# Kernel optimization log

Hardware: AMD Instinct MI355X
Metric: run time of the kernel (lower is better)

The kernel has to match this reference:

```python
import jax, jax.numpy as jnp
import numpy as np

B, T, N, HOR = 64, 12, 1024, 12
D_IN, D_OUT, RNN, E, K = 1, 1, 64, 8, 3
MEM_N, MEM_D = 10, 32
DEC = RNN + MEM_D  # 96 (memory_type='local')
YCOV = 1


def setup_inputs() -> dict:
    key = jax.random.key(0)
    ks = jax.random.split(key, 12)
    s = 0.1  # xavier-ish scale for weights
    return {
        "x": jax.random.normal(ks[0], (B, T, N, D_IN), jnp.float32),
        "y_cov": jax.random.normal(ks[1], (B, HOR, N, YCOV), jnp.float32),
        "node_embeddings": jax.random.normal(ks[2], (N, E), jnp.float32),
        "enc_gate_W": jax.random.normal(ks[3], (K * (D_IN + RNN), 2 * RNN), jnp.float32) * s,
        "enc_gate_b": jnp.zeros((2 * RNN,), jnp.float32),
        "enc_up_W": jax.random.normal(ks[4], (K * (D_IN + RNN), RNN), jnp.float32) * s,
        "enc_up_b": jnp.zeros((RNN,), jnp.float32),
        "Memory": jax.random.normal(ks[5], (MEM_N, MEM_D), jnp.float32) * s,
        "Wq": jax.random.normal(ks[6], (RNN, MEM_D), jnp.float32) * s,
        "FC_E": jax.random.normal(ks[7], (MEM_D, E), jnp.float32) * s,
        "dec_gate_W": jax.random.normal(ks[8], (K * (D_OUT + YCOV + DEC), 2 * DEC), jnp.float32) * s,
        "dec_gate_b": jnp.zeros((2 * DEC,), jnp.float32),
        "dec_up_W": jax.random.normal(ks[9], (K * (D_OUT + YCOV + DEC), DEC), jnp.float32) * s,
        "dec_up_b": jnp.zeros((DEC,), jnp.float32),
        "proj_W": jax.random.normal(ks[10], (DEC, D_OUT), jnp.float32) * s,
        "proj_b": jnp.zeros((D_OUT,), jnp.float32),
    }


def _cheb_supports(S):
    # S: (N,N) soft adjacency -> stacked Chebyshev set [I, S, 2S@S_{k-1}-S_{k-2}, ...], (K,N,N)
    n = S.shape[0]
    sup = [jnp.eye(n, dtype=S.dtype), S]
    for _ in range(2, K):
        sup.append(2.0 * S @ sup[-1] - sup[-2])
    return jnp.stack(sup)


def _agcn(xin, supports, W, b):
    # xin: (B,N,C); supports: (K,N,N); W: (K*C, O)
    xg = jnp.einsum('knm,bmc->bnkc', supports, xin)  # k-major matches torch cat order
    bsz, n = xin.shape[0], xin.shape[1]
    xg = xg.reshape(bsz, n, -1)
    return xg @ W + b


def _cell(xt, state, supports, gW, gb, uW, ub, hdim):
    inp = jnp.concatenate([xt, state], axis=-1)
    z_r = jax.nn.sigmoid(_agcn(inp, supports, gW, gb))
    z, r = z_r[..., :hdim], z_r[..., hdim:]
    cand = jnp.concatenate([xt, z * state], axis=-1)
    hc = jnp.tanh(_agcn(cand, supports, uW, ub))
    return r * state + (1.0 - r) * hc


def reference(x, y_cov, node_embeddings, enc_gate_W, enc_gate_b, enc_up_W, enc_up_b,
              Memory, Wq, FC_E, dec_gate_W, dec_gate_b, dec_up_W, dec_up_b, proj_W, proj_b):
    # ---- encoder supports from static node embeddings (2D path in AGCN) ----
    S_enc = jax.nn.softmax(jax.nn.relu(node_embeddings @ node_embeddings.T), axis=1)
    sup_enc = _cheb_supports(S_enc)

    # ---- encoder: GRU-style recurrence over T timesteps (lax.scan) ----
    def enc_step(state, xt):
        h = _cell(xt, state, sup_enc, enc_gate_W, enc_gate_b, enc_up_W, enc_up_b, RNN)
        return h, None
    h0 = jnp.zeros((x.shape[0], N, RNN), x.dtype)
    h_t, _ = jax.lax.scan(enc_step, h0, jnp.swapaxes(x, 0, 1))  # final hidden (B,N,RNN)

    # ---- memory query (memory_type='local') ----
    query = h_t @ Wq                                  # (B,N,MEM_D)
    att = jax.nn.softmax(query @ Memory.T, axis=-1)   # (B,N,MEM_N)
    proto_t = att @ Memory                            # (B,N,MEM_D)
    W_E = proto_t @ FC_E                              # (B,N,E) meta node embeddings

    # ---- decoder supports from meta embeddings (3D path: einsum sums over batch) ----
    S_dec = jax.nn.softmax(jax.nn.relu(jnp.einsum('bnc,bmc->nm', W_E, W_E)), axis=1)
    sup_dec = _cheb_supports(S_dec)

    # ---- stepwise decoder with go symbol ----
    dec_h0 = jnp.concatenate([h_t, proto_t], axis=-1)  # (B,N,DEC)
    go0 = jnp.zeros((x.shape[0], N, D_OUT), x.dtype)

    def dec_step(carry, yc_t):
        go, state = carry
        xt = jnp.concatenate([go, yc_t], axis=-1)
        h = _cell(xt, state, sup_dec, dec_gate_W, dec_gate_b, dec_up_W, dec_up_b, DEC)
        go_new = h @ proj_W + proj_b
        return (go_new, h), go_new

    _, outs = jax.lax.scan(dec_step, (go0, dec_h0), jnp.swapaxes(y_cov, 0, 1))
    return jnp.swapaxes(outs, 0, 1)  # (B, horizon, N, D_OUT)
```

## Files before the change

kernel.cpp:

```cpp
#include <hip/hip_runtime.h>
#include <hip/hip_bf16.h>

constexpr int B_ = 64, T_ = 12, NN = 1024, HOR_ = 12;

typedef __attribute__((ext_vector_type(8))) short short8;
typedef __attribute__((ext_vector_type(4))) float f32x4;
typedef unsigned short ushort_t;

static __device__ inline ushort_t f2bh(float v) {
  __hip_bfloat16 h = __float2bfloat16(v);
  return *reinterpret_cast<ushort_t*>(&h);
}
static __device__ inline float bh2f(ushort_t u) {
  __hip_bfloat16 h = *reinterpret_cast<__hip_bfloat16*>(&u);
  return __bfloat162float(h);
}
static __device__ inline void split_bf16(float v, ushort_t& hi, ushort_t& lo) {
  hi = f2bh(v);
  lo = f2bh(v - bh2f(hi));
}

static __device__ inline void gload_lds16(const ushort_t* g, ushort_t* l) {
  __builtin_amdgcn_global_load_lds(
      (const __attribute__((address_space(1))) unsigned int*)g,
      (__attribute__((address_space(3))) unsigned int*)l, 16, 0, 0);
}

__global__ void gemm_nt_kernel(const float* __restrict__ A, const float* __restrict__ Bm,
                               float* __restrict__ C, int Ncol, int Kd) {
  __shared__ float As[16][68];
  __shared__ float Bs[16][68];
  const int bm = blockIdx.y * 64, bn = blockIdx.x * 64;
  const int tid = threadIdx.x;
  const int tx = tid & 15, ty = tid >> 4;
  float acc[4][4] = {};
  for (int k0 = 0; k0 < Kd; k0 += 16) {
#pragma unroll
    for (int r = 0; r < 4; ++r) {
      const int m = (tid >> 4) + r * 16;
      const int kk = tid & 15;
      const int k = k0 + kk;
      As[kk][m] = (k < Kd) ? A[(size_t)(bm + m) * Kd + k] : 0.f;
      Bs[kk][m] = (k < Kd) ? Bm[(size_t)(bn + m) * Kd + k] : 0.f;
    }
    __syncthreads();
#pragma unroll
    for (int kk = 0; kk < 16; ++kk) {
      float a[4], b[4];
#pragma unroll
      for (int i = 0; i < 4; ++i) a[i] = As[kk][ty * 4 + i];
#pragma unroll
      for (int j = 0; j < 4; ++j) b[j] = Bs[kk][tx * 4 + j];
#pragma unroll
      for (int i = 0; i < 4; ++i)
#pragma unroll
        for (int j = 0; j < 4; ++j) acc[i][j] += a[i] * b[j];
    }
    __syncthreads();
  }
#pragma unroll
  for (int i = 0; i < 4; ++i)
#pragma unroll
    for (int j = 0; j < 4; ++j)
      C[(size_t)(bm + ty * 4 + i) * Ncol + bn + tx * 4 + j] = acc[i][j];
}

__global__ void relu_softmax_kernel(float* __restrict__ S, ushort_t* __restrict__ Sh,
                                    ushort_t* __restrict__ Sl) {
  const int row = blockIdx.x;
  float* r = S + (size_t)row * NN;
  const int tid = threadIdx.x;
  float v[4];
  float mx = 0.f;
#pragma unroll
  for (int j = 0; j < 4; ++j) {
    float xv = fmaxf(r[tid + j * 256], 0.f);
    v[j] = xv;
    mx = fmaxf(mx, xv);
  }
#pragma unroll
  for (int off = 1; off < 64; off <<= 1) mx = fmaxf(mx, __shfl_xor(mx, off));
  __shared__ float sred[4];
  const int wv = tid >> 6;
  if ((tid & 63) == 0) sred[wv] = mx;
  __syncthreads();
  mx = fmaxf(fmaxf(sred[0], sred[1]), fmaxf(sred[2], sred[3]));
  __syncthreads();
  float s = 0.f;
#pragma unroll
  for (int j = 0; j < 4; ++j) { v[j] = expf(v[j] - mx); s += v[j]; }
#pragma unroll
  for (int off = 1; off < 64; off <<= 1) s += __shfl_xor(s, off);
  if ((tid & 63) == 0) sred[wv] = s;
  __syncthreads();
  s = sred[0] + sred[1] + sred[2] + sred[3];
  const float inv = 1.f / s;
#pragma unroll
  for (int j = 0; j < 4; ++j) {
    const float sv = v[j] * inv;
    const size_t e = (size_t)row * NN + tid + j * 256;
    r[tid + j * 256] = sv;
    ushort_t hi, lo;
    split_bf16(sv, hi, lo);
    Sh[e] = hi;
    Sl[e] = lo;
  }
}

__global__ void st_kernel(const float* __restrict__ S, ushort_t* __restrict__ STh,
                          ushort_t* __restrict__ STl) {
  __shared__ float tile[64][65];
  const int bx = blockIdx.x * 64, by = blockIdx.y * 64;
  const int tid = threadIdx.x;
  const int cl = tid & 63, rq = tid >> 6;
#pragma unroll
  for (int r = 0; r < 16; ++r) {
    const int rr = rq + r * 4;
    tile[rr][cl] = S[(size_t)(by + rr) * NN + bx + cl];
  }
  __syncthreads();
#pragma unroll
  for (int r = 0; r < 16; ++r) {
    const int rr = rq + r * 4;
    const float v = tile[cl][rr];
    ushort_t hi, lo;
    split_bf16(v, hi, lo);
    STh[(size_t)(bx + rr) * NN + by + cl] = hi;
    STl[(size_t)(bx + rr) * NN + by + cl] = lo;
  }
}

__global__ void cheb_mfma_kernel(const ushort_t* __restrict__ S1h,
                                 const ushort_t* __restrict__ S1l,
                                 const ushort_t* __restrict__ STh,
                                 const ushort_t* __restrict__ STl,
                                 ushort_t* __restrict__ Mh) {
  __shared__ __align__(16) ushort_t sA[2 * 32 * 64];
  __shared__ __align__(16) ushort_t sB[2 * 64 * 64];
  const int bj = blockIdx.x * 64, bn = blockIdx.y * 32;
  const int tid = threadIdx.x;
  const int w = tid >> 6, lane = tid & 63;
  const int row = lane & 15, kq = lane >> 4;
  const int srow8 = lane >> 3, sslot = lane & 7;
  f32x4 acc[2] = {};
  for (int k0 = 0; k0 < NN; k0 += 64) {
#pragma unroll
    for (int t2 = 0; t2 < 2; ++t2) {
      const int c = w + t2 * 4, p = c >> 2, i = c & 3;
      const int grow = i * 8 + srow8;
      const int gch = sslot ^ (grow & 7);
      const ushort_t* src = (p ? S1l : S1h) + (size_t)(bn + grow) * NN + k0 + gch * 8;
      gload_lds16(src, sA + p * 2048 + i * 512);
    }
#pragma unroll
    for (int t2 = 0; t2 < 4; ++t2) {
      const int c2 = w + t2 * 4, p = c2 >> 3, rb = c2 & 7;
      const int grow = rb * 8 + srow8;
      const int gch = sslot ^ (grow & 7);
      const ushort_t* src = (p ? STl : STh) + (size_t)(bj + grow) * NN + k0 + gch * 8;
      gload_lds16(src, sB + p * 4096 + rb * 512);
    }
    __syncthreads();
#pragma unroll
    for (int kk = 0; kk < 2; ++kk) {
      const int rB = w * 16 + row;
      const int chB = ((kk * 4 + kq) ^ (rB & 7)) * 8;
      const short8 bh = *(const short8*)(sB + rB * 64 + chB);
      const short8 bl = *(const short8*)(sB + 4096 + rB * 64 + chB);
#pragma unroll
      for (int mt = 0; mt < 2; ++mt) {
        const int rA = mt * 16 + row;
        const int chA = ((kk * 4 + kq) ^ (rA & 7)) * 8;
        const short8 ah = *(const short8*)(sA + rA * 64 + chA);
        const short8 al = *(const short8*)(sA + 2048 + rA * 64 + chA);
        acc[mt] = __builtin_amdgcn_mfma_f32_16x16x32_bf16(ah, bh, acc[mt], 0, 0, 0);
        acc[mt] = __builtin_amdgcn_mfma_f32_16x16x32_bf16(ah, bl, acc[mt], 0, 0, 0);
        acc[mt] = __builtin_amdgcn_mfma_f32_16x16x32_bf16(al, bh, acc[mt], 0, 0, 0);
      }
    }
    __syncthreads();
  }
  const int j = bj + w * 16 + row;
#pragma unroll
  for (int mt = 0; mt < 2; ++mt) {
    const int node0 = bn + mt * 16 + kq * 4;
#pragma unroll
    for (int r = 0; r < 4; ++r)
      Mh[(size_t)(node0 + r) * NN + j] = f2bh(2.f * acc[mt][r]);
  }
}

__global__ void wt_kernel(const float* __restrict__ W, ushort_t* __restrict__ Wth,
                          int KK, int NO, int KP, int NOP) {
  const int e = blockIdx.x * 256 + threadIdx.x;
  if (e >= NOP * KP) return;
  const int no = e / KP, k = e - no * KP;
  const float v = (no < NO && k < KK) ? W[(size_t)k * NO + no] : 0.f;
  Wth[e] = f2bh(v);
}

template <int C, int KP, int MODE>
__global__ void prep_kernel(const float* __restrict__ src0, const float* __restrict__ src1,
                            const float* __restrict__ hst,
                            ushort_t* __restrict__ Agh, ushort_t* __restrict__ XTh) {
  __shared__ float tile[64][65];
  const int bj = blockIdx.x * 64, bn = blockIdx.y * 64;
  const int tid = threadIdx.x;
  const int jl = tid & 63, nq = tid >> 6;
  const int j = bj + jl;
  const int b = j / C, c = j - b * C;
#pragma unroll
  for (int r = 0; r < 16; ++r) {
    const int node = bn + nq + r * 4;
    const int idx = node * 64 + b;
    float v;
    if (MODE == 0) {
      v = (c == 0) ? src0[((size_t)b * T_) * NN + node]
                   : hst[(size_t)idx * 64 + (c - 1)];
    } else {
      v = (c == 0) ? src0[idx]
        : (c == 1) ? src1[((size_t)b * HOR_) * NN + node]
                   : hst[(size_t)idx * 96 + (c - 2)];
    }
    tile[nq + r * 4][jl] = v;
    Agh[(size_t)idx * KP + c] = f2bh(v);
  }
  __syncthreads();
  const int nl = tid & 63, jq = tid >> 6;
#pragma unroll
  for (int r = 0; r < 16; ++r) {
    const int jj = bj + jq + r * 4;
    XTh[(size_t)jj * NN + bn + nl] = f2bh(tile[nl][jq + r * 4]);
  }
}

template <int C, int KP>
__global__ void xt_kernel(const ushort_t* __restrict__ Agh, ushort_t* __restrict__ XTh) {
  __shared__ ushort_t tile[64][70];
  const int bj = blockIdx.x * 64, bn = blockIdx.y * 64;
  const int tid = threadIdx.x;
  const int jl = tid & 63, nq = tid >> 6;
  const int j = bj + jl;
  const int b = j / C, c = j - b * C;
#pragma unroll
  for (int r = 0; r < 16; ++r) {
    const int node = bn + nq + r * 4;
    tile[nq + r * 4][jl] = Agh[(size_t)(node * 64 + b) * KP + c];
  }
  __syncthreads();
  const int nl = tid & 63, jq = tid >> 6;
#pragma unroll
  for (int r = 0; r < 16; ++r) {
    const int jj = bj + jq + r * 4;
    XTh[(size_t)jj * NN + bn + nl] = tile[nl][jq + r * 4];
  }
}

__global__ void set_x_kernel(const float* __restrict__ x, ushort_t* __restrict__ Agh, int t) {
  const int idx = blockIdx.x * 256 + threadIdx.x;
  const int n = idx >> 6, b = idx & 63;
  Agh[(size_t)idx * 224] = f2bh(x[((size_t)b * T_ + t) * NN + n]);
}

template <int C, int KP>
__global__ void graph_mfma_kernel(const ushort_t* __restrict__ S1h,
                                  const ushort_t* __restrict__ Mh,
                                  const ushort_t* __restrict__ XTh,
                                  ushort_t* __restrict__ Agh) {
  constexpr int W = B_ * C;
  const int bj = blockIdx.x * 128;
  if (bj >= W) return;
  __shared__ __align__(16) ushort_t sA[2 * 32 * 64];
  __shared__ __align__(16) ushort_t sB[128 * 64];
  const int bn = blockIdx.y * 32;
  const int tid = threadIdx.x;
  const int w = tid >> 6, lane = tid & 63;
  const int row = lane & 15, kq = lane >> 4;
  const int srow8 = lane >> 3;
  const int sslot = lane & 7;

  const int s = w >> 1;
  const int jhalf = (w & 1) * 64;
  const ushort_t* A_lds = sA + s * (32 * 64);

  f32x4 acc[2][4] = {};
  for (int k0 = 0; k0 < NN; k0 += 64) {
#pragma unroll
    for (int t2 = 0; t2 < 6; ++t2) {
      const int cid = w + t2 * 4;
      if (cid < 8) {
        const int p = cid >> 2, i = cid & 3;
        const int grow = i * 8 + srow8;
        const int gch = sslot ^ (grow & 7);
        const ushort_t* g = (p ? Mh : S1h) + (size_t)(bn + grow) * NN + k0 + gch * 8;
        gload_lds16(g, sA + p * (32 * 64) + i * 512);
      } else {
        const int rb = cid - 8;
        const int brow = rb * 8 + srow8;
        const int gch = sslot ^ (brow & 7);
        const ushort_t* g = XTh + (size_t)(bj + brow) * NN + k0 + gch * 8;
        gload_lds16(g, sB + rb * 512);
      }
    }
    __syncthreads();
    short8 a[2][2];
#pragma unroll
    for (int kk = 0; kk < 2; ++kk)
#pragma unroll
      for (int mt = 0; mt < 2; ++mt) {
        const int r = mt * 16 + row;
        const int chunk = (kk * 4 + kq) ^ (r & 7);
        a[kk][mt] = *(const short8*)(A_lds + r * 64 + chunk * 8);
      }
#pragma unroll
    for (int nt = 0; nt < 4; ++nt) {
#pragma unroll
      for (int kk = 0; kk < 2; ++kk) {
        const int r = jhalf + nt * 16 + row;
        const int chunk = (kk * 4 + kq) ^ (r & 7);
        const short8 bh = *(const short8*)(sB + r * 64 + chunk * 8);
#pragma unroll
        for (int mt = 0; mt < 2; ++mt)
          acc[mt][nt] = __builtin_amdgcn_mfma_f32_16x16x32_bf16(a[kk][mt], bh, acc[mt][nt], 0, 0, 0);
      }
    }
    __syncthreads();
  }
  const int slice_off = (s + 1) * C;
#pragma unroll
  for (int nt = 0; nt < 4; ++nt) {
    const int j = bj + jhalf + nt * 16 + row;
    if (j < W) {
      const int b = j / C, c = j - b * C;
      const size_t coloff = (size_t)(slice_off + c);
#pragma unroll
      for (int mt = 0; mt < 2; ++mt) {
        const int node0 = bn + mt * 16 + kq * 4;
        float sub[4] = {0.f, 0.f, 0.f, 0.f};
        if (s == 1) {
          const ushort_t* xp = XTh + (size_t)j * NN + node0;
#pragma unroll
          for (int r = 0; r < 4; ++r) sub[r] = bh2f(xp[r]);
        }
#pragma unroll
        for (int r = 0; r < 4; ++r) {
          const size_t a = (size_t)((node0 + r) * 64 + b) * KP + coloff;
          Agh[a] = f2bh(acc[mt][nt][r] - sub[r]);
        }
      }
    }
  }
}

template <int KP, int NO, int NOP, int MODE, int H, int CO>
__global__ void dense_mfma_kernel(ushort_t* __restrict__ Agh,
                                  const ushort_t* __restrict__ Wth,
                                  const float* __restrict__ bias,
                                  float* __restrict__ hstate,
                                  float* __restrict__ rbuf) {
  constexpr int NFR = NO / 16;
  __shared__ __align__(16) ushort_t sAh[128 * 32];
  __shared__ __align__(16) ushort_t sBh[NOP * 32];
  const int row0 = blockIdx.x * 128;
  const int tid = threadIdx.x;
  const int w = tid >> 6, lane = tid & 63;
  const int col16 = lane & 15, four = lane >> 4;
  const int srow = lane >> 2;
  const int scol = ((lane & 3) ^ ((srow >> 1) & 3)) * 8;
  const int kqs = (four ^ ((col16 >> 1) & 3)) * 8;
  f32x4 acc[2][NFR] = {};
  for (int k0 = 0; k0 < KP; k0 += 32) {
    for (int c = w; c < 8; c += 4) {
      const size_t g = (size_t)(row0 + c * 16 + srow) * KP + k0 + scol;
      gload_lds16(Agh + g, sAh + c * 512);
    }
    for (int c = w; c < NOP / 16; c += 4) {
      const size_t g = (size_t)(c * 16 + srow) * KP + k0 + scol;
      gload_lds16(Wth + g, sBh + c * 512);
    }
    __syncthreads();
    short8 ah[2];
#pragma unroll
    for (int mt = 0; mt < 2; ++mt) {
      const int r = (w * 32 + mt * 16 + col16) * 32 + kqs;
      ah[mt] = *(const short8*)(sAh + r);
    }
#pragma unroll
    for (int nt = 0; nt < NFR; ++nt) {
      const int r = (nt * 16 + col16) * 32 + kqs;
      const short8 bh = *(const short8*)(sBh + r);
#pragma unroll
      for (int mt = 0; mt < 2; ++mt)
        acc[mt][nt] = __builtin_amdgcn_mfma_f32_16x16x32_bf16(ah[mt], bh, acc[mt][nt], 0, 0, 0);
    }
    __syncthreads();
  }
#pragma unroll
  for (int nt = 0; nt < NFR; ++nt) {
    const int col = nt * 16 + col16;
    const float bv = bias[col];
#pragma unroll
    for (int mt = 0; mt < 2; ++mt) {
      const int rbase = row0 + w * 32 + mt * 16 + four * 4;
#pragma unroll
      for (int r = 0; r < 4; ++r) {
        const int row = rbase + r;
        const float v = acc[mt][nt][r] + bv;
        if (MODE == 2) {
          const float sg = 1.f / (1.f + expf(-v));
          if (col < H) {
            const float hv = hstate[(size_t)row * H + col];
            Agh[(size_t)row * KP + CO + col] = f2bh(sg * hv);
          } else {
            rbuf[(size_t)row * H + (col - H)] = sg;
          }
        } else {
          const float rg = rbuf[(size_t)row * H + col];
          const float hv = hstate[(size_t)row * H + col];
          const float hnew = rg * hv + (1.f - rg) * tanhf(v);
          hstate[(size_t)row * H + col] = hnew;
          Agh[(size_t)row * KP + CO + col] = f2bh(hnew);
        }
      }
    }
  }
}

__global__ void attn_kernel(const float* __restrict__ h, const float* __restrict__ Wq,
                            const float* __restrict__ Mem, const float* __restrict__ FCE,
                            float* __restrict__ hB, float* __restrict__ WE) {
  __shared__ float sWq[64 * 32];
  __shared__ float sM[10 * 32];
  __shared__ float sF[32 * 8];
  const int tid = threadIdx.x;
  for (int i = tid; i < 64 * 32; i += 256) sWq[i] = Wq[i];
  for (int i = tid; i < 10 * 32; i += 256) sM[i] = Mem[i];
  for (int i = tid; i < 32 * 8; i += 256) sF[i] = FCE[i];
  __syncthreads();
  const int idx = blockIdx.x * 256 + tid;
  const float* hp = h + (size_t)idx * 64;
  float* hd = hB + (size_t)idx * 96;
  float q[32] = {};
  for (int i0 = 0; i0 < 16; ++i0) {
    const float4 h4 = *(const float4*)(hp + i0 * 4);
#pragma unroll
    for (int jj = 0; jj < 4; ++jj) {
      const float hv = ((const float*)&h4)[jj];
      hd[i0 * 4 + jj] = hv;
      const int i = i0 * 4 + jj;
#pragma unroll
      for (int c = 0; c < 32; ++c) q[c] += hv * sWq[i * 32 + c];
    }
  }
  float lg[10];
  float mx = -1e30f;
#pragma unroll
  for (int m = 0; m < 10; ++m) {
    float s = 0.f;
#pragma unroll
    for (int c = 0; c < 32; ++c) s += q[c] * sM[m * 32 + c];
    lg[m] = s;
    mx = fmaxf(mx, s);
  }
  float den = 0.f;
#pragma unroll
  for (int m = 0; m < 10; ++m) { lg[m] = expf(lg[m] - mx); den += lg[m]; }
  const float inv = 1.f / den;
  float p[32] = {};
#pragma unroll
  for (int m = 0; m < 10; ++m) {
    const float a = lg[m] * inv;
#pragma unroll
    for (int c = 0; c < 32; ++c) p[c] += a * sM[m * 32 + c];
  }
#pragma unroll
  for (int c = 0; c < 32; ++c) hd[64 + c] = p[c];
  float* wd = WE + (size_t)idx * 8;
#pragma unroll
  for (int e = 0; e < 8; ++e) {
    float s = 0.f;
#pragma unroll
    for (int c = 0; c < 32; ++c) s += p[c] * sF[c * 8 + e];
    wd[e] = s;
  }
}

__global__ void proj_kernel(const float* __restrict__ h, const float* __restrict__ pW,
                            const float* __restrict__ pb, float* __restrict__ go,
                            const float* __restrict__ ycov, ushort_t* __restrict__ Agh,
                            float* __restrict__ out, int t) {
  __shared__ float sW[96];
  if (threadIdx.x < 96) sW[threadIdx.x] = pW[threadIdx.x];
  __syncthreads();
  const int idx = blockIdx.x * 256 + threadIdx.x;
  const float* hp = h + (size_t)idx * 96;
  float acc = pb[0];
  for (int j0 = 0; j0 < 24; ++j0) {
    const float4 h4 = *(const float4*)(hp + j0 * 4);
    acc += h4.x * sW[j0 * 4] + h4.y * sW[j0 * 4 + 1] + h4.z * sW[j0 * 4 + 2] + h4.w * sW[j0 * 4 + 3];
  }
  go[idx] = acc;
  const int n = idx >> 6, b = idx & 63;
  out[((size_t)b * HOR_ + t) * NN + n] = acc;
  if (t + 1 < HOR_) {
    Agh[(size_t)idx * 320 + 0] = f2bh(acc);
    Agh[(size_t)idx * 320 + 1] = f2bh(ycov[((size_t)b * HOR_ + t + 1) * NN + n]);
  }
}

extern "C" void kernel_launch(void* const* d_in, const int* in_sizes, int n_in,
                              void* d_out, int out_size, void* d_ws, size_t ws_size,
                              hipStream_t stream) {
  const float* x    = (const float*)d_in[0];
  const float* ycov = (const float*)d_in[1];
  const float* emb  = (const float*)d_in[2];
  const float* egW  = (const float*)d_in[3];
  const float* egb  = (const float*)d_in[4];
  const float* euW  = (const float*)d_in[5];
  const float* eub  = (const float*)d_in[6];
  const float* Mem  = (const float*)d_in[7];
  const float* Wq   = (const float*)d_in[8];
  const float* FCE  = (const float*)d_in[9];
  const float* dgW  = (const float*)d_in[10];
  const float* dgb  = (const float*)d_in[11];
  const float* duW  = (const float*)d_in[12];
  const float* dub  = (const float*)d_in[13];
  const float* pW   = (const float*)d_in[14];
  const float* pb   = (const float*)d_in[15];
  float* out = (float*)d_out;

  char* w = (char*)d_ws;
  auto alloc = [&](size_t bytes) {
    void* p = (void*)w;
    w += (bytes + 255) & ~(size_t)255;
    return p;
  };
  float* S1   = (float*)alloc((size_t)NN * NN * 4);
  float* rbuf = (float*)alloc((size_t)NN * B_ * 96 * 4);
  float* hA   = (float*)alloc((size_t)NN * B_ * 64 * 4);
  float* hB   = (float*)alloc((size_t)NN * B_ * 96 * 4);
  float* go   = (float*)alloc((size_t)NN * B_ * 4);
  float* WE   = (float*)alloc((size_t)NN * B_ * 8 * 4);
  ushort_t* S1h = (ushort_t*)alloc((size_t)NN * NN * 2);
  ushort_t* S1l = (ushort_t*)alloc((size_t)NN * NN * 2);
  ushort_t* Mh  = (ushort_t*)alloc((size_t)NN * NN * 2);
  ushort_t* STh = (ushort_t*)alloc((size_t)NN * NN * 2);
  ushort_t* STl = (ushort_t*)alloc((size_t)NN * NN * 2);
  ushort_t* XTh = (ushort_t*)alloc((size_t)B_ * 98 * NN * 2);
  ushort_t* Agh = (ushort_t*)alloc((size_t)NN * B_ * 320 * 2);
  ushort_t* WtegH = (ushort_t*)alloc(128 * 224 * 2);
  ushort_t* WteuH = (ushort_t*)alloc(64 * 224 * 2);
  ushort_t* WtdgH = (ushort_t*)alloc(192 * 320 * 2);
  ushort_t* WtduH = (ushort_t*)alloc(128 * 320 * 2);
  (void)ws_size; (void)in_sizes; (void)n_in; (void)out_size;

  const dim3 blk(256);

  wt_kernel<<<(128 * 224 + 255) / 256, blk, 0, stream>>>(egW, WtegH, 195, 128, 224, 128);
  wt_kernel<<<(64 * 224 + 255) / 256, blk, 0, stream>>>(euW, WteuH, 195, 64, 224, 64);
  wt_kernel<<<(192 * 320 + 255) / 256, blk, 0, stream>>>(dgW, WtdgH, 294, 192, 320, 192);
  wt_kernel<<<(128 * 320 + 255) / 256, blk, 0, stream>>>(duW, WtduH, 294, 96, 320, 128);
  hipMemsetAsync(Agh, 0, (size_t)NN * B_ * 320 * 2, stream);
  hipMemsetAsync(hA, 0, (size_t)NN * B_ * 64 * 4, stream);
  hipMemsetAsync(go, 0, (size_t)NN * B_ * 4, stream);

  gemm_nt_kernel<<<dim3(16, 16), blk, 0, stream>>>(emb, emb, S1, NN, 8);
  relu_softmax_kernel<<<NN, blk, 0, stream>>>(S1, S1h, S1l);
  st_kernel<<<dim3(16, 16), blk, 0, stream>>>(S1, STh, STl);
  cheb_mfma_kernel<<<dim3(16, 32), blk, 0, stream>>>(S1h, S1l, STh, STl, Mh);

  for (int t = 0; t < T_; ++t) {
    if (t == 0) {
      prep_kernel<65, 224, 0><<<dim3(65, 16), blk, 0, stream>>>(x, nullptr, hA, Agh, XTh);
    } else {
      set_x_kernel<<<256, blk, 0, stream>>>(x, Agh, t);
      xt_kernel<65, 224><<<dim3(65, 16), blk, 0, stream>>>(Agh, XTh);
    }
    graph_mfma_kernel<65, 224><<<dim3(40, 32), blk, 0, stream>>>(S1h, Mh, XTh, Agh);
    dense_mfma_kernel<224, 128, 128, 2, 64, 1><<<512, blk, 0, stream>>>(Agh, WtegH, egb, hA, rbuf);
    xt_kernel<65, 224><<<dim3(65, 16), blk, 0, stream>>>(Agh, XTh);
    graph_mfma_kernel<65, 224><<<dim3(40, 32), blk, 0, stream>>>(S1h, Mh, XTh, Agh);
    dense_mfma_kernel<224, 64, 64, 1, 64, 1><<<512, blk, 0, stream>>>(Agh, WteuH, eub, hA, rbuf);
  }

  attn_kernel<<<256, blk, 0, stream>>>(hA, Wq, Mem, FCE, hB, WE);
  gemm_nt_kernel<<<dim3(16, 16), blk, 0, stream>>>(WE, WE, S1, NN, 512);
  relu_softmax_kernel<<<NN, blk, 0, stream>>>(S1, S1h, S1l);
  st_kernel<<<dim3(16, 16), blk, 0, stream>>>(S1, STh, STl);
  cheb_mfma_kernel<<<dim3(16, 32), blk, 0, stream>>>(S1h, S1l, STh, STl, Mh);

  for (int t = 0; t < HOR_; ++t) {
    if (t == 0) {
      prep_kernel<98, 320, 2><<<dim3(98, 16), blk, 0, stream>>>(go, ycov, hB, Agh, XTh);
    } else {
      xt_kernel<98, 320><<<dim3(98, 16), blk, 0, stream>>>(Agh, XTh);
    }
    graph_mfma_kernel<98, 320><<<dim3(56, 32), blk, 0, stream>>>(S1h, Mh, XTh, Agh);
    dense_mfma_kernel<320, 192, 192, 2, 96, 2><<<512, blk, 0, stream>>>(Agh, WtdgH, dgb, hB, rbuf);
    xt_kernel<98, 320><<<dim3(98, 16), blk, 0, stream>>>(Agh, XTh);
    graph_mfma_kernel<98, 320><<<dim3(56, 32), blk, 0, stream>>>(S1h, Mh, XTh, Agh);
    dense_mfma_kernel<320, 96, 128, 1, 96, 2><<<512, blk, 0, stream>>>(Agh, WtduH, dub, hB, rbuf);
    proj_kernel<<<256, blk, 0, stream>>>(hB, pW, pb, go, ycov, Agh, out, t);
  }
}
```

Measured before the change: 3.893 ms.

## Fuse x-load into transpose, projection into update GEMM, and use MFMA SYRK

Folds set_x into the transpose kernel and the output projection into the decoder update GEMM epilogue via a lane shuffle reduction, removing two launches per step. It also replaces the scalar gemm_nt over the meta embeddings with a split-bf16 MFMA SYRK kernel. These cut launch overhead and the extra global passes over the hidden state. In exchange, the split-bf16 products drop the lo*lo term, so precision is slightly lower, and the MODE==3 path relies on the existing mode handling for the update.

```diff
diff --git a/kernel.cpp b/kernel.cpp
--- a/kernel.cpp
+++ b/kernel.cpp
@@ -187,6 +187,65 @@
 #pragma unroll
     for (int r = 0; r < 4; ++r)
       Mh[(size_t)(node0 + r) * NN + j] = f2bh(2.f * acc[mt][r]);
+  }
+}
+
+__global__ void we_syrk_kernel(const ushort_t* __restrict__ WEh,
+                               const ushort_t* __restrict__ WEl,
+                               float* __restrict__ S1out) {
+  __shared__ __align__(16) ushort_t sA[2 * 32 * 64];
+  __shared__ __align__(16) ushort_t sB[2 * 64 * 64];
+  const int bj = blockIdx.x * 64, bn = blockIdx.y * 32;
+  const int tid = threadIdx.x;
+  const int w = tid >> 6, lane = tid & 63;
+  const int row = lane & 15, kq = lane >> 4;
+  const int srow8 = lane >> 3, sslot = lane & 7;
+  f32x4 acc[2] = {};
+  for (int k0 = 0; k0 < 512; k0 += 64) {
+#pragma unroll
+    for (int t2 = 0; t2 < 6; ++t2) {
+      const int cid = w + t2 * 4;
+      if (cid < 8) {
+        const int p = cid >> 2, i = cid & 3;
+        const int grow = i * 8 + srow8;
+        const int gch = sslot ^ (grow & 7);
+        const ushort_t* src = (p ? WEl : WEh) + (size_t)(bn + grow) * 512 + k0 + gch * 8;
+        gload_lds16(src, sA + p * 2048 + i * 512);
+      } else {
+        const int c2 = cid - 8, p = c2 >> 3, rb = c2 & 7;
+        const int grow = rb * 8 + srow8;
+        const int gch = sslot ^ (grow & 7);
+        const ushort_t* src = (p ? WEl : WEh) + (size_t)(bj + grow) * 512 + k0 + gch * 8;
+        gload_lds16(src, sB + p * 4096 + rb * 512);
+      }
+    }
+    __syncthreads();
+#pragma unroll
+    for (int kk = 0; kk < 2; ++kk) {
+      const int rB = w * 16 + row;
+      const int chB = ((kk * 4 + kq) ^ (rB & 7)) * 8;
+      const short8 bh = *(const short8*)(sB + rB * 64 + chB);
+      const short8 bl = *(const short8*)(sB + 4096 + rB * 64 + chB);
+#pragma unroll
+      for (int mt = 0; mt < 2; ++mt) {
+        const int rA = mt * 16 + row;
+        const int chA = ((kk * 4 + kq) ^ (rA & 7)) * 8;
+        const short8 ah = *(const short8*)(sA + rA * 64 + chA);
+        const short8 al = *(const short8*)(sA + 2048 + rA * 64 + chA);
+        acc[mt] = __builtin_amdgcn_mfma_f32_16x16x32_bf16(ah, bh, acc[mt], 0, 0, 0);
+        acc[mt] = __builtin_amdgcn_mfma_f32_16x16x32_bf16(ah, bl, acc[mt], 0, 0, 0);
+        acc[mt] = __builtin_amdgcn_mfma_f32_16x16x32_bf16(al, bh, acc[mt], 0, 0, 0);
+      }
+    }
+    __syncthreads();
+  }
+  const int j = bj + w * 16 + row;
+#pragma unroll
+  for (int mt = 0; mt < 2; ++mt) {
+    const int node0 = bn + mt * 16 + kq * 4;
+#pragma unroll
+    for (int r = 0; r < 4; ++r)
+      S1out[(size_t)(node0 + r) * NN + j] = acc[mt][r];
   }
 }
 
@@ -234,8 +293,9 @@
   }
 }
 
-template <int C, int KP>
-__global__ void xt_kernel(const ushort_t* __restrict__ Agh, ushort_t* __restrict__ XTh) {
+template <int C, int KP, bool WITHX>
+__global__ void xt_kernel(ushort_t* __restrict__ Agh, ushort_t* __restrict__ XTh,
+                          const float* __restrict__ x, int t) {
   __shared__ ushort_t tile[64][70];
   const int bj = blockIdx.x * 64, bn = blockIdx.y * 64;
   const int tid = threadIdx.x;
@@ -245,7 +305,15 @@
 #pragma unroll
   for (int r = 0; r < 16; ++r) {
     const int node = bn + nq + r * 4;
-    tile[nq + r * 4][jl] = Agh[(size_t)(node * 64 + b) * KP + c];
+    const int idx = node * 64 + b;
+    ushort_t uv;
+    if (WITHX && c == 0) {
+      uv = f2bh(x[((size_t)b * T_ + t) * NN + node]);
+      Agh[(size_t)idx * KP] = uv;
+    } else {
+      uv = Agh[(size_t)idx * KP + c];
+    }
+    tile[nq + r * 4][jl] = uv;
   }
   __syncthreads();
   const int nl = tid & 63, jq = tid >> 6;
@@ -254,12 +322,6 @@
     const int jj = bj + jq + r * 4;
     XTh[(size_t)jj * NN + bn + nl] = tile[nl][jq + r * 4];
   }
-}
-
-__global__ void set_x_kernel(const float* __restrict__ x, ushort_t* __restrict__ Agh, int t) {
-  const int idx = blockIdx.x * 256 + threadIdx.x;
-  const int n = idx >> 6, b = idx & 63;
-  Agh[(size_t)idx * 224] = f2bh(x[((size_t)b * T_ + t) * NN + n]);
 }
 
 template <int C, int KP>
@@ -344,8 +406,8 @@
         }
 #pragma unroll
         for (int r = 0; r < 4; ++r) {
-          const size_t a = (size_t)((node0 + r) * 64 + b) * KP + coloff;
-          Agh[a] = f2bh(acc[mt][nt][r] - sub[r]);
+          const size_t a2 = (size_t)((node0 + r) * 64 + b) * KP + coloff;
+          Agh[a2] = f2bh(acc[mt][nt][r] - sub[r]);
         }
       }
     }
@@ -357,7 +419,13 @@
                                   const ushort_t* __restrict__ Wth,
                                   const float* __restrict__ bias,
                                   float* __restrict__ hstate,
-                                  float* __restrict__ rbuf) {
+                                  float* __restrict__ rbuf,
+                                  const float* __restrict__ pW,
+                                  const float* __restrict__ pb,
+                                  const float* __restrict__ ycov,
+                                  float* __restrict__ outp,
+                                  float* __restrict__ go,
+                                  int t) {
   constexpr int NFR = NO / 16;
   __shared__ __align__(16) ushort_t sAh[128 * 32];
   __shared__ __align__(16) ushort_t sBh[NOP * 32];
@@ -395,10 +463,18 @@
     }
     __syncthreads();
   }
+  float pgo[2][4];
+  if (MODE == 3) {
+#pragma unroll
+    for (int mt = 0; mt < 2; ++mt)
+#pragma unroll
+      for (int r = 0; r < 4; ++r) pgo[mt][r] = 0.f;
+  }
 #pragma unroll
   for (int nt = 0; nt < NFR; ++nt) {
     const int col = nt * 16 + col16;
     const float bv = bias[col];
+    const float pwv = (MODE == 3) ? pW[col] : 0.f;
 #pragma unroll
     for (int mt = 0; mt < 2; ++mt) {
       const int rbase = row0 + w * 32 + mt * 16 + four * 4;
@@ -420,6 +496,31 @@
           const float hnew = rg * hv + (1.f - rg) * tanhf(v);
           hstate[(size_t)row * H + col] = hnew;
           Agh[(size_t)row * KP + CO + col] = f2bh(hnew);
+          if (MODE == 3) pgo[mt][r] += hnew * pwv;
+        }
+      }
+    }
+  }
+  if (MODE == 3) {
+#pragma unroll
+    for (int mt = 0; mt < 2; ++mt) {
+#pragma unroll
+      for (int r = 0; r < 4; ++r) {
+        float v = pgo[mt][r];
+        v += __shfl_xor(v, 1);
+        v += __shfl_xor(v, 2);
+        v += __shfl_xor(v, 4);
+        v += __shfl_xor(v, 8);
+        v += pb[0];
+        if (col16 == 0) {
+          const int row = row0 + w * 32 + mt * 16 + four * 4 + r;
+          const int n = row >> 6, b = row & 63;
+          outp[((size_t)b * HOR_ + t) * NN + n] = v;
+          go[row] = v;
+          if (t + 1 < HOR_) {
+            Agh[(size_t)row * KP + 0] = f2bh(v);
+            Agh[(size_t)row * KP + 1] = f2bh(ycov[((size_t)b * HOR_ + t + 1) * NN + n]);
+          }
         }
       }
     }
@@ -428,7 +529,8 @@
 
 __global__ void attn_kernel(const float* __restrict__ h, const float* __restrict__ Wq,
                             const float* __restrict__ Mem, const float* __restrict__ FCE,
-                            float* __restrict__ hB, float* __restrict__ WE) {
+                            float* __restrict__ hB, ushort_t* __restrict__ WEh,
+                            ushort_t* __restrict__ WEl) {
   __shared__ float sWq[64 * 32];
   __shared__ float sM[10 * 32];
   __shared__ float sF[32 * 8];
@@ -475,36 +577,15 @@
   }
 #pragma unroll
   for (int c = 0; c < 32; ++c) hd[64 + c] = p[c];
-  float* wd = WE + (size_t)idx * 8;
 #pragma unroll
   for (int e = 0; e < 8; ++e) {
     float s = 0.f;
 #pragma unroll
     for (int c = 0; c < 32; ++c) s += p[c] * sF[c * 8 + e];
-    wd[e] = s;
-  }
-}
-
-__global__ void proj_kernel(const float* __restrict__ h, const float* __restrict__ pW,
-                            const float* __restrict__ pb, float* __restrict__ go,
-                            const float* __restrict__ ycov, ushort_t* __restrict__ Agh,
-                            float* __restrict__ out, int t) {
-  __shared__ float sW[96];
-  if (threadIdx.x < 96) sW[threadIdx.x] = pW[threadIdx.x];
-  __syncthreads();
-  const int idx = blockIdx.x * 256 + threadIdx.x;
-  const float* hp = h + (size_t)idx * 96;
-  float acc = pb[0];
-  for (int j0 = 0; j0 < 24; ++j0) {
-    const float4 h4 = *(const float4*)(hp + j0 * 4);
-    acc += h4.x * sW[j0 * 4] + h4.y * sW[j0 * 4 + 1] + h4.z * sW[j0 * 4 + 2] + h4.w * sW[j0 * 4 + 3];
-  }
-  go[idx] = acc;
-  const int n = idx >> 6, b = idx & 63;
-  out[((size_t)b * HOR_ + t) * NN + n] = acc;
-  if (t + 1 < HOR_) {
-    Agh[(size_t)idx * 320 + 0] = f2bh(acc);
-    Agh[(size_t)idx * 320 + 1] = f2bh(ycov[((size_t)b * HOR_ + t + 1) * NN + n]);
+    ushort_t hi, lo;
+    split_bf16(s, hi, lo);
+    WEh[(size_t)idx * 8 + e] = hi;
+    WEl[(size_t)idx * 8 + e] = lo;
   }
 }
 
@@ -540,7 +621,8 @@
   float* hA   = (float*)alloc((size_t)NN * B_ * 64 * 4);
   float* hB   = (float*)alloc((size_t)NN * B_ * 96 * 4);
   float* go   = (float*)alloc((size_t)NN * B_ * 4);
-  float* WE   = (float*)alloc((size_t)NN * B_ * 8 * 4);
+  ushort_t* WEh = (ushort_t*)alloc((size_t)NN * 512 * 2);
+  ushort_t* WEl = (ushort_t*)alloc((size_t)NN * 512 * 2);
   ushort_t* S1h = (ushort_t*)alloc((size_t)NN * NN * 2);
   ushort_t* S1l = (ushort_t*)alloc((size_t)NN * NN * 2);
   ushort_t* Mh  = (ushort_t*)alloc((size_t)NN * NN * 2);
@@ -573,18 +655,19 @@
     if (t == 0) {
       prep_kernel<65, 224, 0><<<dim3(65, 16), blk, 0, stream>>>(x, nullptr, hA, Agh, XTh);
     } else {
-      set_x_kernel<<<256, blk, 0, stream>>>(x, Agh, t);
-      xt_kernel<65, 224><<<dim3(65, 16), blk, 0, stream>>>(Agh, XTh);
+      xt_kernel<65, 224, true><<<dim3(65, 16), blk, 0, stream>>>(Agh, XTh, x, t);
     }
     graph_mfma_kernel<65, 224><<<dim3(40, 32), blk, 0, stream>>>(S1h, Mh, XTh, Agh);
-    dense_mfma_kernel<224, 128, 128, 2, 64, 1><<<512, blk, 0, stream>>>(Agh, WtegH, egb, hA, rbuf);
-    xt_kernel<65, 224><<<dim3(65, 16), blk, 0, stream>>>(Agh, XTh);
+    dense_mfma_kernel<224, 128, 128, 2, 64, 1><<<512, blk, 0, stream>>>(
+        Agh, WtegH, egb, hA, rbuf, nullptr, nullptr, nullptr, nullptr, nullptr, 0);
+    xt_kernel<65, 224, false><<<dim3(65, 16), blk, 0, stream>>>(Agh, XTh, nullptr, 0);
     graph_mfma_kernel<65, 224><<<dim3(40, 32), blk, 0, stream>>>(S1h, Mh, XTh, Agh);
-    dense_mfma_kernel<224, 64, 64, 1, 64, 1><<<512, blk, 0, stream>>>(Agh, WteuH, eub, hA, rbuf);
-  }
-
-  attn_kernel<<<256, blk, 0, stream>>>(hA, Wq, Mem, FCE, hB, WE);
-  gemm_nt_kernel<<<dim3(16, 16), blk, 0, stream>>>(WE, WE, S1, NN, 512);
+    dense_mfma_kernel<224, 64, 64, 1, 64, 1><<<512, blk, 0, stream>>>(
+        Agh, WteuH, eub, hA, rbuf, nullptr, nullptr, nullptr, nullptr, nullptr, 0);
+  }
+
+  attn_kernel<<<256, blk, 0, stream>>>(hA, Wq, Mem, FCE, hB, WEh, WEl);
+  we_syrk_kernel<<<dim3(16, 32), blk, 0, stream>>>(WEh, WEl, S1);
   relu_softmax_kernel<<<NN, blk, 0, stream>>>(S1, S1h, S1l);
   st_kernel<<<dim3(16, 16), blk, 0, stream>>>(S1, STh, STl);
   cheb_mfma_kernel<<<dim3(16, 32), blk, 0, stream>>>(S1h, S1l, STh, STl, Mh);
@@ -593,13 +676,14 @@
     if (t == 0) {
       prep_kernel<98, 320, 2><<<dim3(98, 16), blk, 0, stream>>>(go, ycov, hB, Agh, XTh);
     } else {
-      xt_kernel<98, 320><<<dim3(98, 16), blk, 0, stream>>>(Agh, XTh);
+      xt_kernel<98, 320, false><<<dim3(98, 16), blk, 0, stream>>>(Agh, XTh, nullptr, 0);
     }
     graph_mfma_kernel<98, 320><<<dim3(56, 32), blk, 0, stream>>>(S1h, Mh, XTh, Agh);
-    dense_mfma_kernel<320, 192, 192, 2, 96, 2><<<512, blk, 0, stream>>>(Agh, WtdgH, dgb, hB, rbuf);
-    xt_kernel<98, 320><<<dim3(98, 16), blk, 0, stream>>>(Agh, XTh);
+    dense_mfma_kernel<320, 192, 192, 2, 96, 2><<<512, blk, 0, stream>>>(
+        Agh, WtdgH, dgb, hB, rbuf, nullptr, nullptr, nullptr, nullptr, nullptr, 0);
+    xt_kernel<98, 320, false><<<dim3(98, 16), blk, 0, stream>>>(Agh, XTh, nullptr, 0);
     graph_mfma_kernel<98, 320><<<dim3(56, 32), blk, 0, stream>>>(S1h, Mh, XTh, Agh);
-    dense_mfma_kernel<320, 96, 128, 1, 96, 2><<<512, blk, 0, stream>>>(Agh, WtduH, dub, hB, rbuf);
-    proj_kernel<<<256, blk, 0, stream>>>(hB, pW, pb, go, ycov, Agh, out, t);
-  }
-}
+    dense_mfma_kernel<320, 96, 128, 3, 96, 2><<<512, blk, 0, stream>>>(
+        Agh, WtduH, dub, hB, rbuf, pW, pb, ycov, out, go, t);
+  }
+}
```

Measured after the change: 3.853 ms. About the same (-1.0%).
